# Kernel tuning notes

Measured on AMD Instinct MI355X. Metric: run time of the kernel, lower is better.

## Reference

```python
import jax, jax.numpy as jnp
import numpy as np

N = 50000      # nodes
E = 800000     # edges (no self loops; module re-adds them)
F_IN = 128     # feats_per_node
H1, C1 = 8, 32     # conv1: heads=8, out=32 -> concat hidden = 256
H2, C2 = 1, 128    # conv2: heads=1, out=128, concat=False (mean)
NEG = 0.2      # leaky relu slope


def _glorot(key, shape):
    fan_in, fan_out = shape[-1], int(np.prod(shape[:-1]))
    lim = float(np.sqrt(6.0 / (fan_in + fan_out)))
    return jax.random.uniform(key, shape, jnp.float32, -lim, lim)


def setup_inputs() -> dict:
    key = jax.random.key(0)
    ks = jax.random.split(key, 10)
    x = jax.random.normal(ks[0], (N, F_IN), jnp.float32)
    src = jax.random.randint(ks[1], (E,), 0, N, dtype=jnp.int32)
    off = jax.random.randint(ks[2], (E,), 1, N, dtype=jnp.int32)
    dst = (src + off) % N  # guarantees src != dst (no self loops)
    edge_index = jnp.stack([src, dst])  # [2, E], row0=source j, row1=target i
    return {
        "x": x,
        "edge_index": edge_index,
        "lin1_w": _glorot(ks[3], (H1 * C1, F_IN)),
        "att1_i": _glorot(ks[4], (1, H1, C1)),
        "att1_j": _glorot(ks[5], (1, H1, C1)),
        "bias1": jnp.zeros((H1 * C1,), jnp.float32),
        "lin2_w": _glorot(ks[6], (C2, H1 * C1)),
        "att2_i": _glorot(ks[7], (1, H2, C2)),
        "att2_j": _glorot(ks[8], (1, H2, C2)),
        "bias2": jnp.zeros((C2,), jnp.float32),
    }


def _gat_conv(x, src, dst, lin_w, att_i, att_j, bias, heads, out_ch, concat):
    n = x.shape[0]
    xh = (x @ lin_w.T).reshape(n, heads, out_ch)          # [n, H, C]
    # add self loops (input edges have none; module removes then adds)
    sl = jnp.arange(n, dtype=src.dtype)
    s = jnp.concatenate([src, sl])
    d = jnp.concatenate([dst, sl])
    # per-node attention logits, then gather per edge (avoids per-edge dot)
    ai = jnp.sum(xh * att_i, axis=-1)                     # [n, H]
    aj = jnp.sum(xh * att_j, axis=-1)                     # [n, H]
    alpha = ai[d] + aj[s]                                 # [Etot, H]
    alpha = jnp.where(alpha > 0, alpha, NEG * alpha)      # leaky relu
    # segment softmax over destination node (every node has a self loop)
    m = jax.ops.segment_max(alpha, d, num_segments=n)
    alpha = jnp.exp(alpha - m[d])
    denom = jax.ops.segment_sum(alpha, d, num_segments=n)
    alpha = alpha / (denom[d] + 1e-16)
    # weighted scatter-add aggregation
    out = jax.ops.segment_sum(xh[s] * alpha[:, :, None], d, num_segments=n)
    out = out.reshape(n, heads * out_ch) if concat else out.mean(axis=1)
    return out + bias


def reference(x, edge_index, lin1_w, att1_i, att1_j, bias1,
              lin2_w, att2_i, att2_j, bias2):
    src, dst = edge_index[0], edge_index[1]
    h = _gat_conv(x, src, dst, lin1_w, att1_i, att1_j, bias1, H1, C1, True)
    h = jax.nn.elu(h)
    return _gat_conv(h, src, dst, lin2_w, att2_i, att2_j, bias2, H2, C2, False)
```

## Files before the change

### kernel.cpp

```cpp
#include <hip/hip_runtime.h>
#include <math.h>

#define NN   50000
#define NE   800000
#define FIN  128
#define HID  256
#define NH1  8
#define C2   128
#define CAP  64
#define NEGS 0.2f

#define NGRP 196
#define CAPB 4608
#define NBIN 782

#define W1R  272
#define W2R  144

typedef __attribute__((ext_vector_type(8))) short bf16x8;
typedef __attribute__((ext_vector_type(4))) float f32x4;

__device__ inline unsigned short f2bf(float f) {
    union { float f; unsigned u; } v; v.f = f;
    unsigned u = v.u;
    u += 0x7fffu + ((u >> 16) & 1u);
    return (unsigned short)(u >> 16);
}
__device__ inline float bf2f(unsigned short h) {
    union { unsigned u; float f; } v; v.u = ((unsigned)h) << 16;
    return v.f;
}

__global__ __launch_bounds__(256) void k_bin(const int* __restrict__ ei,
                                             int* __restrict__ gcnt,
                                             int* __restrict__ gbuf,
                                             const float* __restrict__ w1,
                                             const float* __restrict__ w2,
                                             const float* __restrict__ a1i,
                                             const float* __restrict__ a1j,
                                             const float* __restrict__ a2i,
                                             const float* __restrict__ a2j,
                                             unsigned short* __restrict__ w1e,
                                             unsigned short* __restrict__ w2e) {
    const int B = blockIdx.x, t = threadIdx.x;
    if (B < NBIN) {
        __shared__ int hcnt[NGRP], hbase[NGRP], h2[NGRP];
        for (int k = t; k < NGRP; k += 256) { hcnt[k] = 0; h2[k] = 0; }
        __syncthreads();
        int sv[4], bv[4];
#pragma unroll
        for (int u = 0; u < 4; ++u) {
            const int e = B * 1024 + u * 256 + t;
            if (e < NE) {
                const int s = ei[e], d = ei[NE + e];
                sv[u] = s | ((d & 255) << 16);
                bv[u] = d >> 8;
                atomicAdd(&hcnt[bv[u]], 1);
            } else bv[u] = -1;
        }
        __syncthreads();
        for (int k = t; k < NGRP; k += 256)
            if (hcnt[k]) hbase[k] = atomicAdd(&gcnt[k], hcnt[k]);
        __syncthreads();
#pragma unroll
        for (int u = 0; u < 4; ++u) {
            if (bv[u] >= 0) {
                const int lp = atomicAdd(&h2[bv[u]], 1);
                const int pos = hbase[bv[u]] + lp;
                if (pos < CAPB) gbuf[(size_t)bv[u] * CAPB + pos] = sv[u];
            }
        }
    } else if (B < 1038) {
        const int g = (B - NBIN) * 256 + t;
        if (g < 32768) w1e[g] = f2bf(w1[g]);
        else w2e[g - 32768] = f2bf(w2[g - 32768]);
    } else if (B < 1046) {
        const int g = (B - 1038) * 256 + t;
        const int r = g >> 7, k = g & 127;
        const int h = r & 7;
        const float* att = (r < 8) ? a1i : a1j;
        float s = 0.f;
        for (int c = 0; c < 32; ++c)
            s += att[h * 32 + c] * w1[(h * 32 + c) * FIN + k];
        w1e[(256 + r) * FIN + k] = f2bf(s);
    } else if (B < 1048) {
        const int g = (B - 1046) * 256 + t;
        const int r = g >> 8, k = g & 255;
        const float* att = (r == 0) ? a2i : a2j;
        float s = 0.f;
        for (int c = 0; c < C2; ++c)
            s += att[c] * w2[c * HID + k];
        w2e[(128 + r) * HID + k] = f2bf(s);
    } else {
        const int g = (B - 1048) * 256 + t;
        w2e[130 * HID + g] = 0;
    }
}

__global__ __launch_bounds__(256) void k_build(const int* __restrict__ gcnt,
                                               const int* __restrict__ gbuf,
                                               int* __restrict__ cnt,
                                               int* __restrict__ csr) {
    const int g = blockIdx.x, t = threadIdx.x;
    __shared__ int ccnt[256];
    ccnt[t] = 0;
    __syncthreads();
    const int n = min(gcnt[g], CAPB);
    const int64_t base = (int64_t)g * CAPB;
    for (int k0 = 0; k0 < n; k0 += 1024) {
        int vv[4];
#pragma unroll
        for (int u = 0; u < 4; ++u) {
            const int k = k0 + u * 256 + t;
            vv[u] = (k < n) ? gbuf[base + k] : -1;
        }
#pragma unroll
        for (int u = 0; u < 4; ++u) {
            if (vv[u] >= 0) {
                const int s = vv[u] & 0xffff;
                const int dlow = (vv[u] >> 16) & 0xff;
                const int slot = atomicAdd(&ccnt[dlow], 1);
                if (slot < CAP)
                    csr[((size_t)g * 256 + dlow) * CAP + slot] = s;
            }
        }
    }
    __syncthreads();
    const int node = g * 256 + t;
    if (node < NN) cnt[node] = ccnt[t];
}

__global__ __launch_bounds__(512, 4) void k_gemm1(const float* __restrict__ x,
                                                  const unsigned short* __restrict__ wb,
                                                  unsigned short* __restrict__ xh,
                                                  float* __restrict__ ai,
                                                  float* __restrict__ aj) {
    __shared__ unsigned short wl[W1R * FIN];
    const int t = threadIdx.x;
    for (int idx = t; idx < W1R * 16; idx += 512) {
        const int row = idx >> 4, c = idx & 15;
        *(int4*)((char*)wl + row * 256 + ((c ^ (row & 7)) << 4)) =
            *(const int4*)(wb + row * FIN + c * 8);
    }
    __syncthreads();

    const int w = t >> 6, l = t & 63, m = l & 15, q = l >> 4;
    const int arow = blockIdx.x * 128 + w * 16 + m;
    const int rowc = arow < NN ? arow : NN - 1;

    f32x4 acc[17];
#pragma unroll
    for (int nt = 0; nt < 17; ++nt)
#pragma unroll
        for (int b = 0; b < 4; ++b) acc[nt][b] = 0.f;

#pragma unroll
    for (int ks = 0; ks < 4; ++ks) {
        const int k0 = ks * 32 + q * 8;
        const float4 a0 = *(const float4*)(x + (size_t)rowc * FIN + k0);
        const float4 a1 = *(const float4*)(x + (size_t)rowc * FIN + k0 + 4);
        bf16x8 af;
        af[0] = (short)f2bf(a0.x); af[1] = (short)f2bf(a0.y);
        af[2] = (short)f2bf(a0.z); af[3] = (short)f2bf(a0.w);
        af[4] = (short)f2bf(a1.x); af[5] = (short)f2bf(a1.y);
        af[6] = (short)f2bf(a1.z); af[7] = (short)f2bf(a1.w);
        const int cb = ks * 4 + q;
#pragma unroll
        for (int nt = 0; nt < 17; ++nt) {
            const int n = nt * 16 + m;
            const bf16x8 bf = *(const bf16x8*)((const char*)wl + n * 256 + ((cb ^ (n & 7)) << 4));
            acc[nt] = __builtin_amdgcn_mfma_f32_16x16x32_bf16(af, bf, acc[nt], 0, 0, 0);
        }
    }

    const int orow = blockIdx.x * 128 + w * 16 + 4 * q;
#pragma unroll
    for (int b = 0; b < 4; ++b) {
        if (orow + b >= NN) break;
        unsigned short* dst = xh + (size_t)(orow + b) * HID + m;
#pragma unroll
        for (int nt = 0; nt < 16; ++nt) dst[nt * 16] = f2bf(acc[nt][b]);
        if (m < 8) ai[(orow + b) * NH1 + m]       = acc[16][b];
        else       aj[(orow + b) * NH1 + (m - 8)] = acc[16][b];
    }
}

__global__ __launch_bounds__(256) void k_cvt1(const unsigned short* __restrict__ xh,
                                              unsigned char* __restrict__ xq,
                                              float* __restrict__ scl) {
    const int lane = threadIdx.x & 63;
    const int row  = blockIdx.x * 4 + (threadIdx.x >> 6);
    const ushort4 v = ((const ushort4*)(xh + (size_t)row * HID))[lane];
    const float f0 = bf2f(v.x), f1 = bf2f(v.y), f2 = bf2f(v.z), f3 = bf2f(v.w);
    float m = fmaxf(fmaxf(fabsf(f0), fabsf(f1)), fmaxf(fabsf(f2), fabsf(f3)));
#pragma unroll
    for (int off = 1; off < 64; off <<= 1) m = fmaxf(m, __shfl_xor(m, off, 64));
    m = fmaxf(m, 1e-20f);
    const float inv = 127.f / m;
    const int q0 = (int)rintf(f0 * inv) + 128;
    const int q1 = (int)rintf(f1 * inv) + 128;
    const int q2 = (int)rintf(f2 * inv) + 128;
    const int q3 = (int)rintf(f3 * inv) + 128;
    ((unsigned*)(xq + (size_t)row * HID))[lane] =
        (unsigned)q0 | ((unsigned)q1 << 8) | ((unsigned)q2 << 16) | ((unsigned)q3 << 24);
    if (lane == 0) scl[row] = m * (1.f / 127.f);
}

__global__ __launch_bounds__(256) void k_agg1(const unsigned char* __restrict__ xq,
                                              const float* __restrict__ scl,
                                              const unsigned short* __restrict__ xh,
                                              const float* __restrict__ ai,
                                              const float* __restrict__ aj,
                                              const int* __restrict__ cursor,
                                              const int* __restrict__ csr,
                                              const float* __restrict__ bias,
                                              unsigned short* __restrict__ hout) {
    const int lane = threadIdx.x & 63;
    const int i    = blockIdx.x * 4 + (threadIdx.x >> 6);
    const int sub  = lane & 15;
    const int quad = lane >> 4;
    const int myh  = sub >> 1;
    const float a_i = ai[i * NH1 + myh];

    const int deg = min(cursor[i], CAP);
    const int* rowp = csr + (size_t)i * CAP;
    const int svals = (lane < deg) ? rowp[lane] : i;

    float acc[16];
#pragma unroll
    for (int k = 0; k < 16; ++k) acc[k] = 0.f;
    float dsum = 0.f, wsum = 0.f;

    for (int it = 0; it < deg; it += 8) {
#pragma unroll
        for (int u = 0; u < 2; ++u) {
            const int e = it + u * 4 + quad;
            const int s = __shfl(svals, e & 63, 64);
            float aw = a_i + aj[s * NH1 + myh];
            aw = aw > 0.f ? aw : NEGS * aw;
            const float wv = (e < deg) ? __expf(aw) : 0.f;
            dsum += wv;
            const float wvs = wv * scl[s];
            wsum += wvs;
            const int4 raw = ((const int4*)(xq + (size_t)s * HID))[sub];
            const unsigned dx = (unsigned)raw.x, dy = (unsigned)raw.y;
            const unsigned dz = (unsigned)raw.z, dw = (unsigned)raw.w;
            acc[ 0] += wvs * (float)( dx        & 0xffu);
            acc[ 1] += wvs * (float)((dx >>  8) & 0xffu);
            acc[ 2] += wvs * (float)((dx >> 16) & 0xffu);
            acc[ 3] += wvs * (float)( dx >> 24        );
            acc[ 4] += wvs * (float)( dy        & 0xffu);
            acc[ 5] += wvs * (float)((dy >>  8) & 0xffu);
            acc[ 6] += wvs * (float)((dy >> 16) & 0xffu);
            acc[ 7] += wvs * (float)( dy >> 24        );
            acc[ 8] += wvs * (float)( dz        & 0xffu);
            acc[ 9] += wvs * (float)((dz >>  8) & 0xffu);
            acc[10] += wvs * (float)((dz >> 16) & 0xffu);
            acc[11] += wvs * (float)( dz >> 24        );
            acc[12] += wvs * (float)( dw        & 0xffu);
            acc[13] += wvs * (float)((dw >>  8) & 0xffu);
            acc[14] += wvs * (float)((dw >> 16) & 0xffu);
            acc[15] += wvs * (float)( dw >> 24        );
        }
    }
    dsum += __shfl_xor(dsum, 16, 64);
    dsum += __shfl_xor(dsum, 32, 64);
    wsum += __shfl_xor(wsum, 16, 64);
    wsum += __shfl_xor(wsum, 32, 64);
#pragma unroll
    for (int k = 0; k < 16; ++k) {
        acc[k] += __shfl_xor(acc[k], 16, 64);
        acc[k] += __shfl_xor(acc[k], 32, 64);
    }

    float aws = a_i + aj[i * NH1 + myh];
    aws = aws > 0.f ? aws : NEGS * aws;
    const float wself = __expf(aws);
    dsum += wself;
    const ushort4 sv = *(const ushort4*)(xh + (size_t)i * HID + sub * 16 + quad * 4);

    const float inv = 1.f / (dsum + 1e-16f);
    const float c128 = 128.f * wsum;
    const float4 b = ((const float4*)bias)[sub * 4 + quad];
    float4 o;
    o.x = (acc[quad * 4 + 0] - c128 + wself * bf2f(sv.x)) * inv + b.x;
    o.y = (acc[quad * 4 + 1] - c128 + wself * bf2f(sv.y)) * inv + b.y;
    o.z = (acc[quad * 4 + 2] - c128 + wself * bf2f(sv.z)) * inv + b.z;
    o.w = (acc[quad * 4 + 3] - c128 + wself * bf2f(sv.w)) * inv + b.w;
    o.x = o.x > 0.f ? o.x : expm1f(o.x);
    o.y = o.y > 0.f ? o.y : expm1f(o.y);
    o.z = o.z > 0.f ? o.z : expm1f(o.z);
    o.w = o.w > 0.f ? o.w : expm1f(o.w);
    ushort4 ov;
    ov.x = f2bf(o.x); ov.y = f2bf(o.y); ov.z = f2bf(o.z); ov.w = f2bf(o.w);
    ((ushort4*)(hout + (size_t)i * HID))[sub * 4 + quad] = ov;
}

__global__ __launch_bounds__(512, 4) void k_gemm2(const unsigned short* __restrict__ h1,
                                                  const unsigned short* __restrict__ wb,
                                                  unsigned short* __restrict__ xh2,
                                                  float* __restrict__ ai2,
                                                  float* __restrict__ aj2) {
    __shared__ unsigned short wl[W2R * HID];
    const int t = threadIdx.x;
    for (int idx = t; idx < W2R * 32; idx += 512) {
        const int row = idx >> 5, c = idx & 31;
        *(int4*)((char*)wl + row * 512 + ((c ^ (row & 7)) << 4)) =
            *(const int4*)(wb + row * HID + c * 8);
    }
    __syncthreads();

    const int w = t >> 6, l = t & 63, m = l & 15, q = l >> 4;
    const int arow = blockIdx.x * 128 + w * 16 + m;
    const int rowc = arow < NN ? arow : NN - 1;

    f32x4 acc[9];
#pragma unroll
    for (int nt = 0; nt < 9; ++nt)
#pragma unroll
        for (int b = 0; b < 4; ++b) acc[nt][b] = 0.f;

#pragma unroll
    for (int ks = 0; ks < 8; ++ks) {
        const int k0 = ks * 32 + q * 8;
        const bf16x8 af = *(const bf16x8*)(h1 + (size_t)rowc * HID + k0);
        const int cb = ks * 4 + q;
#pragma unroll
        for (int nt = 0; nt < 9; ++nt) {
            const int n = nt * 16 + m;
            const bf16x8 bf = *(const bf16x8*)((const char*)wl + n * 512 + ((cb ^ (n & 7)) << 4));
            acc[nt] = __builtin_amdgcn_mfma_f32_16x16x32_bf16(af, bf, acc[nt], 0, 0, 0);
        }
    }

    const int orow = blockIdx.x * 128 + w * 16 + 4 * q;
#pragma unroll
    for (int b = 0; b < 4; ++b) {
        if (orow + b >= NN) break;
        unsigned short* dst = xh2 + (size_t)(orow + b) * C2 + m;
#pragma unroll
        for (int nt = 0; nt < 8; ++nt) dst[nt * 16] = f2bf(acc[nt][b]);
        if (m == 0) ai2[orow + b] = acc[8][b];
        if (m == 1) aj2[orow + b] = acc[8][b];
    }
}

__global__ __launch_bounds__(256) void k_cvt2(const unsigned short* __restrict__ xh2,
                                              unsigned char* __restrict__ xq2,
                                              float* __restrict__ scl2) {
    const int lane = threadIdx.x & 63;
    const int row  = blockIdx.x * 4 + (threadIdx.x >> 6);
    const ushort2 v = ((const ushort2*)(xh2 + (size_t)row * C2))[lane];
    const float f0 = bf2f(v.x), f1 = bf2f(v.y);
    float m = fmaxf(fabsf(f0), fabsf(f1));
#pragma unroll
    for (int off = 1; off < 64; off <<= 1) m = fmaxf(m, __shfl_xor(m, off, 64));
    m = fmaxf(m, 1e-20f);
    const float inv = 127.f / m;
    const int q0 = (int)rintf(f0 * inv) + 128;
    const int q1 = (int)rintf(f1 * inv) + 128;
    ((unsigned short*)(xq2 + (size_t)row * C2))[lane] =
        (unsigned short)(q0 | (q1 << 8));
    if (lane == 0) scl2[row] = m * (1.f / 127.f);
}

__global__ __launch_bounds__(256) void k_agg2(const unsigned char* __restrict__ xq2,
                                              const float* __restrict__ scl2,
                                              const unsigned short* __restrict__ xh2,
                                              const float* __restrict__ ai2v,
                                              const float* __restrict__ aj2v,
                                              const int* __restrict__ cursor,
                                              const int* __restrict__ csr,
                                              const float* __restrict__ bias,
                                              float* __restrict__ out) {
    const int lane = threadIdx.x & 63;
    const int i    = blockIdx.x * 4 + (threadIdx.x >> 6);
    const int sub  = lane & 7;
    const int oct  = lane >> 3;
    const float a_i = ai2v[i];

    const int deg = min(cursor[i], CAP);
    const int* rowp = csr + (size_t)i * CAP;
    const int svals = (lane < deg) ? rowp[lane] : i;

    float acc[16];
#pragma unroll
    for (int k = 0; k < 16; ++k) acc[k] = 0.f;
    float dsum = 0.f, wsum = 0.f;

    for (int it = 0; it < deg; it += 16) {
#pragma unroll
        for (int u = 0; u < 2; ++u) {
            const int e = it + u * 8 + oct;
            const int s = __shfl(svals, e & 63, 64);
            float aw = a_i + aj2v[s];
            aw = aw > 0.f ? aw : NEGS * aw;
            const float wv = (e < deg) ? __expf(aw) : 0.f;
            dsum += wv;
            const float wvs = wv * scl2[s];
            wsum += wvs;
            const int4 raw = ((const int4*)(xq2 + (size_t)s * C2))[sub];
            const unsigned dx = (unsigned)raw.x, dy = (unsigned)raw.y;
            const unsigned dz = (unsigned)raw.z, dw = (unsigned)raw.w;
            acc[ 0] += wvs * (float)( dx        & 0xffu);
            acc[ 1] += wvs * (float)((dx >>  8) & 0xffu);
            acc[ 2] += wvs * (float)((dx >> 16) & 0xffu);
            acc[ 3] += wvs * (float)( dx >> 24        );
            acc[ 4] += wvs * (float)( dy        & 0xffu);
            acc[ 5] += wvs * (float)((dy >>  8) & 0xffu);
            acc[ 6] += wvs * (float)((dy >> 16) & 0xffu);
            acc[ 7] += wvs * (float)( dy >> 24        );
            acc[ 8] += wvs * (float)( dz        & 0xffu);
            acc[ 9] += wvs * (float)((dz >>  8) & 0xffu);
            acc[10] += wvs * (float)((dz >> 16) & 0xffu);
            acc[11] += wvs * (float)( dz >> 24        );
            acc[12] += wvs * (float)( dw        & 0xffu);
            acc[13] += wvs * (float)((dw >>  8) & 0xffu);
            acc[14] += wvs * (float)((dw >> 16) & 0xffu);
            acc[15] += wvs * (float)( dw >> 24        );
        }
    }
    dsum += __shfl_xor(dsum, 8, 64);
    dsum += __shfl_xor(dsum, 16, 64);
    dsum += __shfl_xor(dsum, 32, 64);
    wsum += __shfl_xor(wsum, 8, 64);
    wsum += __shfl_xor(wsum, 16, 64);
    wsum += __shfl_xor(wsum, 32, 64);
#pragma unroll
    for (int k = 0; k < 16; ++k) {
        acc[k] += __shfl_xor(acc[k], 8, 64);
        acc[k] += __shfl_xor(acc[k], 16, 64);
        acc[k] += __shfl_xor(acc[k], 32, 64);
    }

    float aws = a_i + aj2v[i];
    aws = aws > 0.f ? aws : NEGS * aws;
    const float wself = __expf(aws);
    dsum += wself;
    const ushort2 sv = *(const ushort2*)(xh2 + (size_t)i * C2 + sub * 16 + oct * 2);

    const float inv = 1.f / (dsum + 1e-16f);
    const float c128 = 128.f * wsum;
    const float2 b = ((const float2*)bias)[sub * 8 + oct];
    float2 o;
    o.x = (acc[oct * 2 + 0] - c128 + wself * bf2f(sv.x)) * inv + b.x;
    o.y = (acc[oct * 2 + 1] - c128 + wself * bf2f(sv.y)) * inv + b.y;
    ((float2*)(out + (size_t)i * C2))[sub * 8 + oct] = o;
}

extern "C" void kernel_launch(void* const* d_in, const int* in_sizes, int n_in,
                              void* d_out, int out_size, void* d_ws, size_t ws_size,
                              hipStream_t stream) {
    const float* x      = (const float*)d_in[0];
    const int*   ei     = (const int*)  d_in[1];
    const float* lin1_w = (const float*)d_in[2];
    const float* att1_i = (const float*)d_in[3];
    const float* att1_j = (const float*)d_in[4];
    const float* bias1  = (const float*)d_in[5];
    const float* lin2_w = (const float*)d_in[6];
    const float* att2_i = (const float*)d_in[7];
    const float* att2_j = (const float*)d_in[8];
    const float* bias2  = (const float*)d_in[9];
    float* out = (float*)d_out;

    char* wsb = (char*)d_ws;
    size_t off = 0;
    auto alloc = [&](size_t bytes) -> void* {
        void* p = wsb + off;
        off += (bytes + 255) & ~(size_t)255;
        return p;
    };
    int*            gcnt   = (int*)           alloc((size_t)NGRP * 4);
    int*            gbuf   = (int*)           alloc((size_t)NGRP * CAPB * 4);
    int*            cnt    = (int*)           alloc((size_t)NN * 4);
    int*            csr    = (int*)           alloc((size_t)NN * CAP * 4);
    unsigned short* w1e    = (unsigned short*)alloc((size_t)W1R * FIN * 2);
    unsigned short* w2e    = (unsigned short*)alloc((size_t)W2R * HID * 2);
    unsigned short* xh1    = (unsigned short*)alloc((size_t)NN * HID * 2);
    unsigned char*  xq1    = (unsigned char*) alloc((size_t)NN * HID);
    float*          scl1   = (float*)         alloc((size_t)NN * 4);
    float*          ai1    = (float*)         alloc((size_t)NN * NH1 * 4);
    float*          aj1    = (float*)         alloc((size_t)NN * NH1 * 4);
    unsigned short* h1     = (unsigned short*)alloc((size_t)NN * HID * 2);
    unsigned short* xh2    = (unsigned short*)alloc((size_t)NN * C2 * 2);
    unsigned char*  xq2    = (unsigned char*) alloc((size_t)NN * C2);
    float*          scl2   = (float*)         alloc((size_t)NN * 4);
    float*          ai2    = (float*)         alloc((size_t)NN * 4);
    float*          aj2    = (float*)         alloc((size_t)NN * 4);
    if (off > ws_size) return;

    const int gm = (NN + 127) / 128;
    hipMemsetAsync(gcnt, 0, (size_t)NGRP * 4, stream);
    k_bin<<<1062, 256, 0, stream>>>(ei, gcnt, gbuf, lin1_w, lin2_w,
                                    att1_i, att1_j, att2_i, att2_j, w1e, w2e);
    k_build<<<NGRP, 256, 0, stream>>>(gcnt, gbuf, cnt, csr);
    k_gemm1<<<gm, 512, 0, stream>>>(x, w1e, xh1, ai1, aj1);
    k_cvt1<<<NN / 4, 256, 0, stream>>>(xh1, xq1, scl1);
    k_agg1<<<NN / 4, 256, 0, stream>>>(xq1, scl1, xh1, ai1, aj1, cnt, csr, bias1, h1);
    k_gemm2<<<gm, 512, 0, stream>>>(h1, w2e, xh2, ai2, aj2);
    k_cvt2<<<NN / 4, 256, 0, stream>>>(xh2, xq2, scl2);
    k_agg2<<<NN / 4, 256, 0, stream>>>(xq2, scl2, xh2, ai2, aj2, cnt, csr, bias2, out);
}
```

Measured before the change: 169.3 us.

## Fuse int8 quantization into GEMM epilogues and precompute per-edge attention weights in LDS

The two GEMM kernels now remap their output columns so each lane holds a contiguous slice of a row. The epilogue then computes the row max, the bf16 copy and the int8 quantization in place, which removes the separate k_cvt1/k_cvt2 passes and their extra read of xh. The aggregation kernels compute the exp attention weights per edge once, all heads at once, and store them in shared memory, so the inner loop no longer does redundant gathers and exps. The inner loop also uses packed two-wide FMAs. The costs are LDS use, a new swizzle to avoid bank conflicts, and more register pressure in the GEMM epilogue.

```diff
diff --git a/kernel.cpp b/kernel.cpp
--- a/kernel.cpp
+++ b/kernel.cpp
@@ -17,8 +17,11 @@
 #define W1R  272
 #define W2R  144
 
+#define SWZ(n) ((((n) & 7)) ^ (((n) >> 4) & 7))
+
 typedef __attribute__((ext_vector_type(8))) short bf16x8;
 typedef __attribute__((ext_vector_type(4))) float f32x4;
+typedef __attribute__((ext_vector_type(2))) float f32x2;
 
 __device__ inline unsigned short f2bf(float f) {
     union { float f; unsigned u; } v; v.f = f;
@@ -133,13 +136,15 @@
 __global__ __launch_bounds__(512, 4) void k_gemm1(const float* __restrict__ x,
                                                   const unsigned short* __restrict__ wb,
                                                   unsigned short* __restrict__ xh,
+                                                  unsigned char* __restrict__ xq,
+                                                  float* __restrict__ scl,
                                                   float* __restrict__ ai,
                                                   float* __restrict__ aj) {
     __shared__ unsigned short wl[W1R * FIN];
     const int t = threadIdx.x;
     for (int idx = t; idx < W1R * 16; idx += 512) {
         const int row = idx >> 4, c = idx & 15;
-        *(int4*)((char*)wl + row * 256 + ((c ^ (row & 7)) << 4)) =
+        *(int4*)((char*)wl + row * 256 + ((c ^ SWZ(row)) << 4)) =
             *(const int4*)(wb + row * FIN + c * 8);
     }
     __syncthreads();
@@ -167,8 +172,8 @@
         const int cb = ks * 4 + q;
 #pragma unroll
         for (int nt = 0; nt < 17; ++nt) {
-            const int n = nt * 16 + m;
-            const bf16x8 bf = *(const bf16x8*)((const char*)wl + n * 256 + ((cb ^ (n & 7)) << 4));
+            const int n = (nt < 16) ? (m * 16 + nt) : (256 + m);
+            const bf16x8 bf = *(const bf16x8*)((const char*)wl + n * 256 + ((cb ^ SWZ(n)) << 4));
             acc[nt] = __builtin_amdgcn_mfma_f32_16x16x32_bf16(af, bf, acc[nt], 0, 0, 0);
         }
     }
@@ -177,33 +182,34 @@
 #pragma unroll
     for (int b = 0; b < 4; ++b) {
         if (orow + b >= NN) break;
-        unsigned short* dst = xh + (size_t)(orow + b) * HID + m;
-#pragma unroll
-        for (int nt = 0; nt < 16; ++nt) dst[nt * 16] = f2bf(acc[nt][b]);
-        if (m < 8) ai[(orow + b) * NH1 + m]       = acc[16][b];
-        else       aj[(orow + b) * NH1 + (m - 8)] = acc[16][b];
-    }
-}
-
-__global__ __launch_bounds__(256) void k_cvt1(const unsigned short* __restrict__ xh,
-                                              unsigned char* __restrict__ xq,
-                                              float* __restrict__ scl) {
-    const int lane = threadIdx.x & 63;
-    const int row  = blockIdx.x * 4 + (threadIdx.x >> 6);
-    const ushort4 v = ((const ushort4*)(xh + (size_t)row * HID))[lane];
-    const float f0 = bf2f(v.x), f1 = bf2f(v.y), f2 = bf2f(v.z), f3 = bf2f(v.w);
-    float m = fmaxf(fmaxf(fabsf(f0), fabsf(f1)), fmaxf(fabsf(f2), fabsf(f3)));
-#pragma unroll
-    for (int off = 1; off < 64; off <<= 1) m = fmaxf(m, __shfl_xor(m, off, 64));
-    m = fmaxf(m, 1e-20f);
-    const float inv = 127.f / m;
-    const int q0 = (int)rintf(f0 * inv) + 128;
-    const int q1 = (int)rintf(f1 * inv) + 128;
-    const int q2 = (int)rintf(f2 * inv) + 128;
-    const int q3 = (int)rintf(f3 * inv) + 128;
-    ((unsigned*)(xq + (size_t)row * HID))[lane] =
-        (unsigned)q0 | ((unsigned)q1 << 8) | ((unsigned)q2 << 16) | ((unsigned)q3 << 24);
-    if (lane == 0) scl[row] = m * (1.f / 127.f);
+        const int row = orow + b;
+        float mx = 1e-20f;
+#pragma unroll
+        for (int nt = 0; nt < 16; ++nt) mx = fmaxf(mx, fabsf(acc[nt][b]));
+#pragma unroll
+        for (int off = 1; off < 16; off <<= 1) mx = fmaxf(mx, __shfl_xor(mx, off, 16));
+        const float qsc = 127.f / mx;
+        unsigned bw[8];
+#pragma unroll
+        for (int k = 0; k < 8; ++k)
+            bw[k] = (unsigned)f2bf(acc[2 * k][b]) | ((unsigned)f2bf(acc[2 * k + 1][b]) << 16);
+        int4* bd = (int4*)(xh + (size_t)row * HID + m * 16);
+        bd[0] = make_int4(bw[0], bw[1], bw[2], bw[3]);
+        bd[1] = make_int4(bw[4], bw[5], bw[6], bw[7]);
+        unsigned qw[4];
+#pragma unroll
+        for (int k = 0; k < 4; ++k) {
+            const int q0 = (int)rintf(acc[4 * k + 0][b] * qsc) + 128;
+            const int q1 = (int)rintf(acc[4 * k + 1][b] * qsc) + 128;
+            const int q2 = (int)rintf(acc[4 * k + 2][b] * qsc) + 128;
+            const int q3 = (int)rintf(acc[4 * k + 3][b] * qsc) + 128;
+            qw[k] = (unsigned)q0 | ((unsigned)q1 << 8) | ((unsigned)q2 << 16) | ((unsigned)q3 << 24);
+        }
+        *(int4*)(xq + (size_t)row * HID + m * 16) = make_int4(qw[0], qw[1], qw[2], qw[3]);
+        if (m == 0) scl[row] = mx * (1.f / 127.f);
+        if (m < 8) ai[row * NH1 + m]       = acc[16][b];
+        else       aj[row * NH1 + (m - 8)] = acc[16][b];
+    }
 }
 
 __global__ __launch_bounds__(256) void k_agg1(const unsigned char* __restrict__ xq,
@@ -211,24 +217,49 @@
                                               const unsigned short* __restrict__ xh,
                                               const float* __restrict__ ai,
                                               const float* __restrict__ aj,
-                                              const int* __restrict__ cursor,
+                                              const int* __restrict__ cnt,
                                               const int* __restrict__ csr,
                                               const float* __restrict__ bias,
                                               unsigned short* __restrict__ hout) {
+    __shared__ float2 psh[4][80 * 8];
+    const int wid  = threadIdx.x >> 6;
     const int lane = threadIdx.x & 63;
-    const int i    = blockIdx.x * 4 + (threadIdx.x >> 6);
+    const int i    = blockIdx.x * 4 + wid;
     const int sub  = lane & 15;
     const int quad = lane >> 4;
     const int myh  = sub >> 1;
-    const float a_i = ai[i * NH1 + myh];
-
-    const int deg = min(cursor[i], CAP);
+
+    const int deg = min(cnt[i], CAP);
     const int* rowp = csr + (size_t)i * CAP;
     const int svals = (lane < deg) ? rowp[lane] : i;
 
-    float acc[16];
-#pragma unroll
-    for (int k = 0; k < 16; ++k) acc[k] = 0.f;
+    float2* wl = psh[wid];
+    {
+        const float4 ai0 = ((const float4*)ai)[i * 2];
+        const float4 ai1 = ((const float4*)ai)[i * 2 + 1];
+        const float4 aj0 = ((const float4*)aj)[svals * 2];
+        const float4 aj1 = ((const float4*)aj)[svals * 2 + 1];
+        const float sc = scl[svals];
+        const float vm = (lane < deg) ? 1.f : 0.f;
+        float a, wv;
+        a = ai0.x + aj0.x; a = a > 0.f ? a : NEGS * a; wv = vm * __expf(a); wl[lane * 8 + 0] = make_float2(wv, wv * sc);
+        a = ai0.y + aj0.y; a = a > 0.f ? a : NEGS * a; wv = vm * __expf(a); wl[lane * 8 + 1] = make_float2(wv, wv * sc);
+        a = ai0.z + aj0.z; a = a > 0.f ? a : NEGS * a; wv = vm * __expf(a); wl[lane * 8 + 2] = make_float2(wv, wv * sc);
+        a = ai0.w + aj0.w; a = a > 0.f ? a : NEGS * a; wv = vm * __expf(a); wl[lane * 8 + 3] = make_float2(wv, wv * sc);
+        a = ai1.x + aj1.x; a = a > 0.f ? a : NEGS * a; wv = vm * __expf(a); wl[lane * 8 + 4] = make_float2(wv, wv * sc);
+        a = ai1.y + aj1.y; a = a > 0.f ? a : NEGS * a; wv = vm * __expf(a); wl[lane * 8 + 5] = make_float2(wv, wv * sc);
+        a = ai1.z + aj1.z; a = a > 0.f ? a : NEGS * a; wv = vm * __expf(a); wl[lane * 8 + 6] = make_float2(wv, wv * sc);
+        a = ai1.w + aj1.w; a = a > 0.f ? a : NEGS * a; wv = vm * __expf(a); wl[lane * 8 + 7] = make_float2(wv, wv * sc);
+        if (lane < 16) {
+            float2* zp = wl + (64 + lane) * 8;
+#pragma unroll
+            for (int h = 0; h < 8; ++h) zp[h] = make_float2(0.f, 0.f);
+        }
+    }
+
+    f32x2 acc2[8];
+#pragma unroll
+    for (int k = 0; k < 8; ++k) acc2[k] = (f32x2){0.f, 0.f};
     float dsum = 0.f, wsum = 0.f;
 
     for (int it = 0; it < deg; it += 8) {
@@ -236,44 +267,37 @@
         for (int u = 0; u < 2; ++u) {
             const int e = it + u * 4 + quad;
             const int s = __shfl(svals, e & 63, 64);
-            float aw = a_i + aj[s * NH1 + myh];
-            aw = aw > 0.f ? aw : NEGS * aw;
-            const float wv = (e < deg) ? __expf(aw) : 0.f;
-            dsum += wv;
-            const float wvs = wv * scl[s];
-            wsum += wvs;
+            const float2 wp = wl[e * 8 + myh];
+            dsum += wp.x; wsum += wp.y;
+            const f32x2 pv = {wp.y, wp.y};
             const int4 raw = ((const int4*)(xq + (size_t)s * HID))[sub];
             const unsigned dx = (unsigned)raw.x, dy = (unsigned)raw.y;
             const unsigned dz = (unsigned)raw.z, dw = (unsigned)raw.w;
-            acc[ 0] += wvs * (float)( dx        & 0xffu);
-            acc[ 1] += wvs * (float)((dx >>  8) & 0xffu);
-            acc[ 2] += wvs * (float)((dx >> 16) & 0xffu);
-            acc[ 3] += wvs * (float)( dx >> 24        );
-            acc[ 4] += wvs * (float)( dy        & 0xffu);
-            acc[ 5] += wvs * (float)((dy >>  8) & 0xffu);
-            acc[ 6] += wvs * (float)((dy >> 16) & 0xffu);
-            acc[ 7] += wvs * (float)( dy >> 24        );
-            acc[ 8] += wvs * (float)( dz        & 0xffu);
-            acc[ 9] += wvs * (float)((dz >>  8) & 0xffu);
-            acc[10] += wvs * (float)((dz >> 16) & 0xffu);
-            acc[11] += wvs * (float)( dz >> 24        );
-            acc[12] += wvs * (float)( dw        & 0xffu);
-            acc[13] += wvs * (float)((dw >>  8) & 0xffu);
-            acc[14] += wvs * (float)((dw >> 16) & 0xffu);
-            acc[15] += wvs * (float)( dw >> 24        );
+            f32x2 d;
+            d = (f32x2){(float)(dx & 0xffu), (float)((dx >> 8) & 0xffu)};   acc2[0] = pv * d + acc2[0];
+            d = (f32x2){(float)((dx >> 16) & 0xffu), (float)(dx >> 24)};   acc2[1] = pv * d + acc2[1];
+            d = (f32x2){(float)(dy & 0xffu), (float)((dy >> 8) & 0xffu)};   acc2[2] = pv * d + acc2[2];
+            d = (f32x2){(float)((dy >> 16) & 0xffu), (float)(dy >> 24)};   acc2[3] = pv * d + acc2[3];
+            d = (f32x2){(float)(dz & 0xffu), (float)((dz >> 8) & 0xffu)};   acc2[4] = pv * d + acc2[4];
+            d = (f32x2){(float)((dz >> 16) & 0xffu), (float)(dz >> 24)};   acc2[5] = pv * d + acc2[5];
+            d = (f32x2){(float)(dw & 0xffu), (float)((dw >> 8) & 0xffu)};   acc2[6] = pv * d + acc2[6];
+            d = (f32x2){(float)((dw >> 16) & 0xffu), (float)(dw >> 24)};   acc2[7] = pv * d + acc2[7];
         }
     }
     dsum += __shfl_xor(dsum, 16, 64);
     dsum += __shfl_xor(dsum, 32, 64);
     wsum += __shfl_xor(wsum, 16, 64);
     wsum += __shfl_xor(wsum, 32, 64);
-#pragma unroll
-    for (int k = 0; k < 16; ++k) {
-        acc[k] += __shfl_xor(acc[k], 16, 64);
-        acc[k] += __shfl_xor(acc[k], 32, 64);
-    }
-
-    float aws = a_i + aj[i * NH1 + myh];
+    float accf[16];
+#pragma unroll
+    for (int k = 0; k < 8; ++k) {
+        float x0 = acc2[k].x, x1 = acc2[k].y;
+        x0 += __shfl_xor(x0, 16, 64); x0 += __shfl_xor(x0, 32, 64);
+        x1 += __shfl_xor(x1, 16, 64); x1 += __shfl_xor(x1, 32, 64);
+        accf[2 * k] = x0; accf[2 * k + 1] = x1;
+    }
+
+    float aws = ai[i * NH1 + myh] + aj[i * NH1 + myh];
     aws = aws > 0.f ? aws : NEGS * aws;
     const float wself = __expf(aws);
     dsum += wself;
@@ -283,10 +307,10 @@
     const float c128 = 128.f * wsum;
     const float4 b = ((const float4*)bias)[sub * 4 + quad];
     float4 o;
-    o.x = (acc[quad * 4 + 0] - c128 + wself * bf2f(sv.x)) * inv + b.x;
-    o.y = (acc[quad * 4 + 1] - c128 + wself * bf2f(sv.y)) * inv + b.y;
-    o.z = (acc[quad * 4 + 2] - c128 + wself * bf2f(sv.z)) * inv + b.z;
-    o.w = (acc[quad * 4 + 3] - c128 + wself * bf2f(sv.w)) * inv + b.w;
+    o.x = (accf[quad * 4 + 0] - c128 + wself * bf2f(sv.x)) * inv + b.x;
+    o.y = (accf[quad * 4 + 1] - c128 + wself * bf2f(sv.y)) * inv + b.y;
+    o.z = (accf[quad * 4 + 2] - c128 + wself * bf2f(sv.z)) * inv + b.z;
+    o.w = (accf[quad * 4 + 3] - c128 + wself * bf2f(sv.w)) * inv + b.w;
     o.x = o.x > 0.f ? o.x : expm1f(o.x);
     o.y = o.y > 0.f ? o.y : expm1f(o.y);
     o.z = o.z > 0.f ? o.z : expm1f(o.z);
@@ -299,13 +323,15 @@
 __global__ __launch_bounds__(512, 4) void k_gemm2(const unsigned short* __restrict__ h1,
                                                   const unsigned short* __restrict__ wb,
                                                   unsigned short* __restrict__ xh2,
+                                                  unsigned char* __restrict__ xq2,
+                                                  float* __restrict__ scl2,
                                                   float* __restrict__ ai2,
                                                   float* __restrict__ aj2) {
     __shared__ unsigned short wl[W2R * HID];
     const int t = threadIdx.x;
     for (int idx = t; idx < W2R * 32; idx += 512) {
         const int row = idx >> 5, c = idx & 31;
-        *(int4*)((char*)wl + row * 512 + ((c ^ (row & 7)) << 4)) =
+        *(int4*)((char*)wl + row * 512 + ((c ^ SWZ(row)) << 4)) =
             *(const int4*)(wb + row * HID + c * 8);
     }
     __syncthreads();
@@ -327,8 +353,8 @@
         const int cb = ks * 4 + q;
 #pragma unroll
         for (int nt = 0; nt < 9; ++nt) {
-            const int n = nt * 16 + m;
-            const bf16x8 bf = *(const bf16x8*)((const char*)wl + n * 512 + ((cb ^ (n & 7)) << 4));
+            const int n = (nt < 8) ? (m * 8 + nt) : (128 + m);
+            const bf16x8 bf = *(const bf16x8*)((const char*)wl + n * 512 + ((cb ^ SWZ(n)) << 4));
             acc[nt] = __builtin_amdgcn_mfma_f32_16x16x32_bf16(af, bf, acc[nt], 0, 0, 0);
         }
     }
@@ -337,31 +363,32 @@
 #pragma unroll
     for (int b = 0; b < 4; ++b) {
         if (orow + b >= NN) break;
-        unsigned short* dst = xh2 + (size_t)(orow + b) * C2 + m;
-#pragma unroll
-        for (int nt = 0; nt < 8; ++nt) dst[nt * 16] = f2bf(acc[nt][b]);
-        if (m == 0) ai2[orow + b] = acc[8][b];
-        if (m == 1) aj2[orow + b] = acc[8][b];
-    }
-}
-
-__global__ __launch_bounds__(256) void k_cvt2(const unsigned short* __restrict__ xh2,
-                                              unsigned char* __restrict__ xq2,
-                                              float* __restrict__ scl2) {
-    const int lane = threadIdx.x & 63;
-    const int row  = blockIdx.x * 4 + (threadIdx.x >> 6);
-    const ushort2 v = ((const ushort2*)(xh2 + (size_t)row * C2))[lane];
-    const float f0 = bf2f(v.x), f1 = bf2f(v.y);
-    float m = fmaxf(fabsf(f0), fabsf(f1));
-#pragma unroll
-    for (int off = 1; off < 64; off <<= 1) m = fmaxf(m, __shfl_xor(m, off, 64));
-    m = fmaxf(m, 1e-20f);
-    const float inv = 127.f / m;
-    const int q0 = (int)rintf(f0 * inv) + 128;
-    const int q1 = (int)rintf(f1 * inv) + 128;
-    ((unsigned short*)(xq2 + (size_t)row * C2))[lane] =
-        (unsigned short)(q0 | (q1 << 8));
-    if (lane == 0) scl2[row] = m * (1.f / 127.f);
+        const int row = orow + b;
+        float mx = 1e-20f;
+#pragma unroll
+        for (int nt = 0; nt < 8; ++nt) mx = fmaxf(mx, fabsf(acc[nt][b]));
+#pragma unroll
+        for (int off = 1; off < 16; off <<= 1) mx = fmaxf(mx, __shfl_xor(mx, off, 16));
+        const float qsc = 127.f / mx;
+        unsigned bw[4];
+#pragma unroll
+        for (int k = 0; k < 4; ++k)
+            bw[k] = (unsigned)f2bf(acc[2 * k][b]) | ((unsigned)f2bf(acc[2 * k + 1][b]) << 16);
+        *(int4*)(xh2 + (size_t)row * C2 + m * 8) = make_int4(bw[0], bw[1], bw[2], bw[3]);
+        unsigned qw[2];
+#pragma unroll
+        for (int k = 0; k < 2; ++k) {
+            const int q0 = (int)rintf(acc[4 * k + 0][b] * qsc) + 128;
+            const int q1 = (int)rintf(acc[4 * k + 1][b] * qsc) + 128;
+            const int q2 = (int)rintf(acc[4 * k + 2][b] * qsc) + 128;
+            const int q3 = (int)rintf(acc[4 * k + 3][b] * qsc) + 128;
+            qw[k] = (unsigned)q0 | ((unsigned)q1 << 8) | ((unsigned)q2 << 16) | ((unsigned)q3 << 24);
+        }
+        *(int2*)(xq2 + (size_t)row * C2 + m * 8) = make_int2(qw[0], qw[1]);
+        if (m == 0) scl2[row] = mx * (1.f / 127.f);
+        if (m == 0) ai2[row] = acc[8][b];
+        if (m == 1) aj2[row] = acc[8][b];
+    }
 }
 
 __global__ __launch_bounds__(256) void k_agg2(const unsigned char* __restrict__ xq2,
@@ -369,23 +396,34 @@
                                               const unsigned short* __restrict__ xh2,
                                               const float* __restrict__ ai2v,
                                               const float* __restrict__ aj2v,
-                                              const int* __restrict__ cursor,
+                                              const int* __restrict__ cnt,
                                               const int* __restrict__ csr,
                                               const float* __restrict__ bias,
                                               float* __restrict__ out) {
+    __shared__ float2 psh[4][80];
+    const int wid  = threadIdx.x >> 6;
     const int lane = threadIdx.x & 63;
-    const int i    = blockIdx.x * 4 + (threadIdx.x >> 6);
+    const int i    = blockIdx.x * 4 + wid;
     const int sub  = lane & 7;
     const int oct  = lane >> 3;
     const float a_i = ai2v[i];
 
-    const int deg = min(cursor[i], CAP);
+    const int deg = min(cnt[i], CAP);
     const int* rowp = csr + (size_t)i * CAP;
     const int svals = (lane < deg) ? rowp[lane] : i;
 
-    float acc[16];
-#pragma unroll
-    for (int k = 0; k < 16; ++k) acc[k] = 0.f;
+    float2* wl = psh[wid];
+    {
+        float a = a_i + aj2v[svals];
+        a = a > 0.f ? a : NEGS * a;
+        const float wv = (lane < deg) ? __expf(a) : 0.f;
+        wl[lane] = make_float2(wv, wv * scl2[svals]);
+        if (lane < 16) wl[64 + lane] = make_float2(0.f, 0.f);
+    }
+
+    f32x2 acc2[8];
+#pragma unroll
+    for (int k = 0; k < 8; ++k) acc2[k] = (f32x2){0.f, 0.f};
     float dsum = 0.f, wsum = 0.f;
 
     for (int it = 0; it < deg; it += 16) {
@@ -393,31 +431,21 @@
         for (int u = 0; u < 2; ++u) {
             const int e = it + u * 8 + oct;
             const int s = __shfl(svals, e & 63, 64);
-            float aw = a_i + aj2v[s];
-            aw = aw > 0.f ? aw : NEGS * aw;
-            const float wv = (e < deg) ? __expf(aw) : 0.f;
-            dsum += wv;
-            const float wvs = wv * scl2[s];
-            wsum += wvs;
+            const float2 wp = wl[e];
+            dsum += wp.x; wsum += wp.y;
+            const f32x2 pv = {wp.y, wp.y};
             const int4 raw = ((const int4*)(xq2 + (size_t)s * C2))[sub];
             const unsigned dx = (unsigned)raw.x, dy = (unsigned)raw.y;
             const unsigned dz = (unsigned)raw.z, dw = (unsigned)raw.w;
-            acc[ 0] += wvs * (float)( dx        & 0xffu);
-            acc[ 1] += wvs * (float)((dx >>  8) & 0xffu);
-            acc[ 2] += wvs * (float)((dx >> 16) & 0xffu);
-            acc[ 3] += wvs * (float)( dx >> 24        );
-            acc[ 4] += wvs * (float)( dy        & 0xffu);
-            acc[ 5] += wvs * (float)((dy >>  8) & 0xffu);
-            acc[ 6] += wvs * (float)((dy >> 16) & 0xffu);
-            acc[ 7] += wvs * (float)( dy >> 24        );
-            acc[ 8] += wvs * (float)( dz        & 0xffu);
-            acc[ 9] += wvs * (float)((dz >>  8) & 0xffu);
-            acc[10] += wvs * (float)((dz >> 16) & 0xffu);
-            acc[11] += wvs * (float)( dz >> 24        );
-            acc[12] += wvs * (float)( dw        & 0xffu);
-            acc[13] += wvs * (float)((dw >>  8) & 0xffu);
-            acc[14] += wvs * (float)((dw >> 16) & 0xffu);
-            acc[15] += wvs * (float)( dw >> 24        );
+            f32x2 d;
+            d = (f32x2){(float)(dx & 0xffu), (float)((dx >> 8) & 0xffu)};   acc2[0] = pv * d + acc2[0];
+            d = (f32x2){(float)((dx >> 16) & 0xffu), (float)(dx >> 24)};   acc2[1] = pv * d + acc2[1];
+            d = (f32x2){(float)(dy & 0xffu), (float)((dy >> 8) & 0xffu)};   acc2[2] = pv * d + acc2[2];
+            d = (f32x2){(float)((dy >> 16) & 0xffu), (float)(dy >> 24)};   acc2[3] = pv * d + acc2[3];
+            d = (f32x2){(float)(dz & 0xffu), (float)((dz >> 8) & 0xffu)};   acc2[4] = pv * d + acc2[4];
+            d = (f32x2){(float)((dz >> 16) & 0xffu), (float)(dz >> 24)};   acc2[5] = pv * d + acc2[5];
+            d = (f32x2){(float)(dw & 0xffu), (float)((dw >> 8) & 0xffu)};   acc2[6] = pv * d + acc2[6];
+            d = (f32x2){(float)((dw >> 16) & 0xffu), (float)(dw >> 24)};   acc2[7] = pv * d + acc2[7];
         }
     }
     dsum += __shfl_xor(dsum, 8, 64);
@@ -426,11 +454,13 @@
     wsum += __shfl_xor(wsum, 8, 64);
     wsum += __shfl_xor(wsum, 16, 64);
     wsum += __shfl_xor(wsum, 32, 64);
-#pragma unroll
-    for (int k = 0; k < 16; ++k) {
-        acc[k] += __shfl_xor(acc[k], 8, 64);
-        acc[k] += __shfl_xor(acc[k], 16, 64);
-        acc[k] += __shfl_xor(acc[k], 32, 64);
+    float accf[16];
+#pragma unroll
+    for (int k = 0; k < 8; ++k) {
+        float x0 = acc2[k].x, x1 = acc2[k].y;
+        x0 += __shfl_xor(x0, 8, 64); x0 += __shfl_xor(x0, 16, 64); x0 += __shfl_xor(x0, 32, 64);
+        x1 += __shfl_xor(x1, 8, 64); x1 += __shfl_xor(x1, 16, 64); x1 += __shfl_xor(x1, 32, 64);
+        accf[2 * k] = x0; accf[2 * k + 1] = x1;
     }
 
     float aws = a_i + aj2v[i];
@@ -443,8 +473,8 @@
     const float c128 = 128.f * wsum;
     const float2 b = ((const float2*)bias)[sub * 8 + oct];
     float2 o;
-    o.x = (acc[oct * 2 + 0] - c128 + wself * bf2f(sv.x)) * inv + b.x;
-    o.y = (acc[oct * 2 + 1] - c128 + wself * bf2f(sv.y)) * inv + b.y;
+    o.x = (accf[oct * 2 + 0] - c128 + wself * bf2f(sv.x)) * inv + b.x;
+    o.y = (accf[oct * 2 + 1] - c128 + wself * bf2f(sv.y)) * inv + b.y;
     ((float2*)(out + (size_t)i * C2))[sub * 8 + oct] = o;
 }
 
@@ -494,10 +524,8 @@
     k_bin<<<1062, 256, 0, stream>>>(ei, gcnt, gbuf, lin1_w, lin2_w,
                                     att1_i, att1_j, att2_i, att2_j, w1e, w2e);
     k_build<<<NGRP, 256, 0, stream>>>(gcnt, gbuf, cnt, csr);
-    k_gemm1<<<gm, 512, 0, stream>>>(x, w1e, xh1, ai1, aj1);
-    k_cvt1<<<NN / 4, 256, 0, stream>>>(xh1, xq1, scl1);
+    k_gemm1<<<gm, 512, 0, stream>>>(x, w1e, xh1, xq1, scl1, ai1, aj1);
     k_agg1<<<NN / 4, 256, 0, stream>>>(xq1, scl1, xh1, ai1, aj1, cnt, csr, bias1, h1);
-    k_gemm2<<<gm, 512, 0, stream>>>(h1, w2e, xh2, ai2, aj2);
-    k_cvt2<<<NN / 4, 256, 0, stream>>>(xh2, xq2, scl2);
+    k_gemm2<<<gm, 512, 0, stream>>>(h1, w2e, xh2, xq2, scl2, ai2, aj2);
     k_agg2<<<NN / 4, 256, 0, stream>>>(xq2, scl2, xh2, ai2, aj2, cnt, csr, bias2, out);
 }
```

Measured after the change: 179.9 us. 6.3% more time.

## Fuse int8 row quantization into GEMM epilogues and remap output columns

Applied to the files above, without the earlier changes.

Folds the separate per-row int8 quantization kernels (k_cvt1, k_cvt2) into the epilogues of both GEMMs. The B-column mapping is permuted so that each lane owns a contiguous 16- or 8-wide chunk of the output row, which allows vectorized int4 stores of bf16 and int8 data. The swizzle is extended to keep LDS reads free of bank conflicts under the new mapping. This removes two kernel launches and a full re-read of the bf16 features, at the cost of more epilogue work and register pressure in the GEMM kernels.

```diff
diff --git a/kernel.cpp b/kernel.cpp
--- a/kernel.cpp
+++ b/kernel.cpp
@@ -16,6 +16,8 @@
 
 #define W1R  272
 #define W2R  144
+
+#define SWZ(n) ((((n) & 7)) ^ (((n) >> 4) & 7))
 
 typedef __attribute__((ext_vector_type(8))) short bf16x8;
 typedef __attribute__((ext_vector_type(4))) float f32x4;
@@ -133,13 +135,15 @@
 __global__ __launch_bounds__(512, 4) void k_gemm1(const float* __restrict__ x,
                                                   const unsigned short* __restrict__ wb,
                                                   unsigned short* __restrict__ xh,
+                                                  unsigned char* __restrict__ xq,
+                                                  float* __restrict__ scl,
                                                   float* __restrict__ ai,
                                                   float* __restrict__ aj) {
     __shared__ unsigned short wl[W1R * FIN];
     const int t = threadIdx.x;
     for (int idx = t; idx < W1R * 16; idx += 512) {
         const int row = idx >> 4, c = idx & 15;
-        *(int4*)((char*)wl + row * 256 + ((c ^ (row & 7)) << 4)) =
+        *(int4*)((char*)wl + row * 256 + ((c ^ SWZ(row)) << 4)) =
             *(const int4*)(wb + row * FIN + c * 8);
     }
     __syncthreads();
@@ -167,8 +171,8 @@
         const int cb = ks * 4 + q;
 #pragma unroll
         for (int nt = 0; nt < 17; ++nt) {
-            const int n = nt * 16 + m;
-            const bf16x8 bf = *(const bf16x8*)((const char*)wl + n * 256 + ((cb ^ (n & 7)) << 4));
+            const int n = (nt < 16) ? (m * 16 + nt) : (256 + m);
+            const bf16x8 bf = *(const bf16x8*)((const char*)wl + n * 256 + ((cb ^ SWZ(n)) << 4));
             acc[nt] = __builtin_amdgcn_mfma_f32_16x16x32_bf16(af, bf, acc[nt], 0, 0, 0);
         }
     }
@@ -177,33 +181,34 @@
 #pragma unroll
     for (int b = 0; b < 4; ++b) {
         if (orow + b >= NN) break;
-        unsigned short* dst = xh + (size_t)(orow + b) * HID + m;
-#pragma unroll
-        for (int nt = 0; nt < 16; ++nt) dst[nt * 16] = f2bf(acc[nt][b]);
-        if (m < 8) ai[(orow + b) * NH1 + m]       = acc[16][b];
-        else       aj[(orow + b) * NH1 + (m - 8)] = acc[16][b];
-    }
-}
-
-__global__ __launch_bounds__(256) void k_cvt1(const unsigned short* __restrict__ xh,
-                                              unsigned char* __restrict__ xq,
-                                              float* __restrict__ scl) {
-    const int lane = threadIdx.x & 63;
-    const int row  = blockIdx.x * 4 + (threadIdx.x >> 6);
-    const ushort4 v = ((const ushort4*)(xh + (size_t)row * HID))[lane];
-    const float f0 = bf2f(v.x), f1 = bf2f(v.y), f2 = bf2f(v.z), f3 = bf2f(v.w);
-    float m = fmaxf(fmaxf(fabsf(f0), fabsf(f1)), fmaxf(fabsf(f2), fabsf(f3)));
-#pragma unroll
-    for (int off = 1; off < 64; off <<= 1) m = fmaxf(m, __shfl_xor(m, off, 64));
-    m = fmaxf(m, 1e-20f);
-    const float inv = 127.f / m;
-    const int q0 = (int)rintf(f0 * inv) + 128;
-    const int q1 = (int)rintf(f1 * inv) + 128;
-    const int q2 = (int)rintf(f2 * inv) + 128;
-    const int q3 = (int)rintf(f3 * inv) + 128;
-    ((unsigned*)(xq + (size_t)row * HID))[lane] =
-        (unsigned)q0 | ((unsigned)q1 << 8) | ((unsigned)q2 << 16) | ((unsigned)q3 << 24);
-    if (lane == 0) scl[row] = m * (1.f / 127.f);
+        const int row = orow + b;
+        float mx = 1e-20f;
+#pragma unroll
+        for (int nt = 0; nt < 16; ++nt) mx = fmaxf(mx, fabsf(acc[nt][b]));
+#pragma unroll
+        for (int off = 1; off < 16; off <<= 1) mx = fmaxf(mx, __shfl_xor(mx, off, 16));
+        const float qsc = 127.f / mx;
+        unsigned bw[8];
+#pragma unroll
+        for (int k = 0; k < 8; ++k)
+            bw[k] = (unsigned)f2bf(acc[2 * k][b]) | ((unsigned)f2bf(acc[2 * k + 1][b]) << 16);
+        int4* bd = (int4*)(xh + (size_t)row * HID + m * 16);
+        bd[0] = make_int4(bw[0], bw[1], bw[2], bw[3]);
+        bd[1] = make_int4(bw[4], bw[5], bw[6], bw[7]);
+        unsigned qw[4];
+#pragma unroll
+        for (int k = 0; k < 4; ++k) {
+            const int q0 = (int)rintf(acc[4 * k + 0][b] * qsc) + 128;
+            const int q1 = (int)rintf(acc[4 * k + 1][b] * qsc) + 128;
+            const int q2 = (int)rintf(acc[4 * k + 2][b] * qsc) + 128;
+            const int q3 = (int)rintf(acc[4 * k + 3][b] * qsc) + 128;
+            qw[k] = (unsigned)q0 | ((unsigned)q1 << 8) | ((unsigned)q2 << 16) | ((unsigned)q3 << 24);
+        }
+        *(int4*)(xq + (size_t)row * HID + m * 16) = make_int4(qw[0], qw[1], qw[2], qw[3]);
+        if (m == 0) scl[row] = mx * (1.f / 127.f);
+        if (m < 8) ai[row * NH1 + m]       = acc[16][b];
+        else       aj[row * NH1 + (m - 8)] = acc[16][b];
+    }
 }
 
 __global__ __launch_bounds__(256) void k_agg1(const unsigned char* __restrict__ xq,
@@ -211,7 +216,7 @@
                                               const unsigned short* __restrict__ xh,
                                               const float* __restrict__ ai,
                                               const float* __restrict__ aj,
-                                              const int* __restrict__ cursor,
+                                              const int* __restrict__ cnt,
                                               const int* __restrict__ csr,
                                               const float* __restrict__ bias,
                                               unsigned short* __restrict__ hout) {
@@ -222,7 +227,7 @@
     const int myh  = sub >> 1;
     const float a_i = ai[i * NH1 + myh];
 
-    const int deg = min(cursor[i], CAP);
+    const int deg = min(cnt[i], CAP);
     const int* rowp = csr + (size_t)i * CAP;
     const int svals = (lane < deg) ? rowp[lane] : i;
 
@@ -299,13 +304,15 @@
 __global__ __launch_bounds__(512, 4) void k_gemm2(const unsigned short* __restrict__ h1,
                                                   const unsigned short* __restrict__ wb,
                                                   unsigned short* __restrict__ xh2,
+                                                  unsigned char* __restrict__ xq2,
+                                                  float* __restrict__ scl2,
                                                   float* __restrict__ ai2,
                                                   float* __restrict__ aj2) {
     __shared__ unsigned short wl[W2R * HID];
     const int t = threadIdx.x;
     for (int idx = t; idx < W2R * 32; idx += 512) {
         const int row = idx >> 5, c = idx & 31;
-        *(int4*)((char*)wl + row * 512 + ((c ^ (row & 7)) << 4)) =
+        *(int4*)((char*)wl + row * 512 + ((c ^ SWZ(row)) << 4)) =
             *(const int4*)(wb + row * HID + c * 8);
     }
     __syncthreads();
@@ -327,8 +334,8 @@
         const int cb = ks * 4 + q;
 #pragma unroll
         for (int nt = 0; nt < 9; ++nt) {
-            const int n = nt * 16 + m;
-            const bf16x8 bf = *(const bf16x8*)((const char*)wl + n * 512 + ((cb ^ (n & 7)) << 4));
+            const int n = (nt < 8) ? (m * 8 + nt) : (128 + m);
+            const bf16x8 bf = *(const bf16x8*)((const char*)wl + n * 512 + ((cb ^ SWZ(n)) << 4));
             acc[nt] = __builtin_amdgcn_mfma_f32_16x16x32_bf16(af, bf, acc[nt], 0, 0, 0);
         }
     }
@@ -337,31 +344,32 @@
 #pragma unroll
     for (int b = 0; b < 4; ++b) {
         if (orow + b >= NN) break;
-        unsigned short* dst = xh2 + (size_t)(orow + b) * C2 + m;
-#pragma unroll
-        for (int nt = 0; nt < 8; ++nt) dst[nt * 16] = f2bf(acc[nt][b]);
-        if (m == 0) ai2[orow + b] = acc[8][b];
-        if (m == 1) aj2[orow + b] = acc[8][b];
-    }
-}
-
-__global__ __launch_bounds__(256) void k_cvt2(const unsigned short* __restrict__ xh2,
-                                              unsigned char* __restrict__ xq2,
-                                              float* __restrict__ scl2) {
-    const int lane = threadIdx.x & 63;
-    const int row  = blockIdx.x * 4 + (threadIdx.x >> 6);
-    const ushort2 v = ((const ushort2*)(xh2 + (size_t)row * C2))[lane];
-    const float f0 = bf2f(v.x), f1 = bf2f(v.y);
-    float m = fmaxf(fabsf(f0), fabsf(f1));
-#pragma unroll
-    for (int off = 1; off < 64; off <<= 1) m = fmaxf(m, __shfl_xor(m, off, 64));
-    m = fmaxf(m, 1e-20f);
-    const float inv = 127.f / m;
-    const int q0 = (int)rintf(f0 * inv) + 128;
-    const int q1 = (int)rintf(f1 * inv) + 128;
-    ((unsigned short*)(xq2 + (size_t)row * C2))[lane] =
-        (unsigned short)(q0 | (q1 << 8));
-    if (lane == 0) scl2[row] = m * (1.f / 127.f);
+        const int row = orow + b;
+        float mx = 1e-20f;
+#pragma unroll
+        for (int nt = 0; nt < 8; ++nt) mx = fmaxf(mx, fabsf(acc[nt][b]));
+#pragma unroll
+        for (int off = 1; off < 16; off <<= 1) mx = fmaxf(mx, __shfl_xor(mx, off, 16));
+        const float qsc = 127.f / mx;
+        unsigned bw[4];
+#pragma unroll
+        for (int k = 0; k < 4; ++k)
+            bw[k] = (unsigned)f2bf(acc[2 * k][b]) | ((unsigned)f2bf(acc[2 * k + 1][b]) << 16);
+        *(int4*)(xh2 + (size_t)row * C2 + m * 8) = make_int4(bw[0], bw[1], bw[2], bw[3]);
+        unsigned qw[2];
+#pragma unroll
+        for (int k = 0; k < 2; ++k) {
+            const int q0 = (int)rintf(acc[4 * k + 0][b] * qsc) + 128;
+            const int q1 = (int)rintf(acc[4 * k + 1][b] * qsc) + 128;
+            const int q2 = (int)rintf(acc[4 * k + 2][b] * qsc) + 128;
+            const int q3 = (int)rintf(acc[4 * k + 3][b] * qsc) + 128;
+            qw[k] = (unsigned)q0 | ((unsigned)q1 << 8) | ((unsigned)q2 << 16) | ((unsigned)q3 << 24);
+        }
+        *(int2*)(xq2 + (size_t)row * C2 + m * 8) = make_int2(qw[0], qw[1]);
+        if (m == 0) scl2[row] = mx * (1.f / 127.f);
+        if (m == 0) ai2[row] = acc[8][b];
+        if (m == 1) aj2[row] = acc[8][b];
+    }
 }
 
 __global__ __launch_bounds__(256) void k_agg2(const unsigned char* __restrict__ xq2,
@@ -369,7 +377,7 @@
                                               const unsigned short* __restrict__ xh2,
                                               const float* __restrict__ ai2v,
                                               const float* __restrict__ aj2v,
-                                              const int* __restrict__ cursor,
+                                              const int* __restrict__ cnt,
                                               const int* __restrict__ csr,
                                               const float* __restrict__ bias,
                                               float* __restrict__ out) {
@@ -379,7 +387,7 @@
     const int oct  = lane >> 3;
     const float a_i = ai2v[i];
 
-    const int deg = min(cursor[i], CAP);
+    const int deg = min(cnt[i], CAP);
     const int* rowp = csr + (size_t)i * CAP;
     const int svals = (lane < deg) ? rowp[lane] : i;
 
@@ -494,10 +502,8 @@
     k_bin<<<1062, 256, 0, stream>>>(ei, gcnt, gbuf, lin1_w, lin2_w,
                                     att1_i, att1_j, att2_i, att2_j, w1e, w2e);
     k_build<<<NGRP, 256, 0, stream>>>(gcnt, gbuf, cnt, csr);
-    k_gemm1<<<gm, 512, 0, stream>>>(x, w1e, xh1, ai1, aj1);
-    k_cvt1<<<NN / 4, 256, 0, stream>>>(xh1, xq1, scl1);
+    k_gemm1<<<gm, 512, 0, stream>>>(x, w1e, xh1, xq1, scl1, ai1, aj1);
     k_agg1<<<NN / 4, 256, 0, stream>>>(xq1, scl1, xh1, ai1, aj1, cnt, csr, bias1, h1);
-    k_gemm2<<<gm, 512, 0, stream>>>(h1, w2e, xh2, ai2, aj2);
-    k_cvt2<<<NN / 4, 256, 0, stream>>>(xh2, xq2, scl2);
+    k_gemm2<<<gm, 512, 0, stream>>>(h1, w2e, xh2, xq2, scl2, ai2, aj2);
     k_agg2<<<NN / 4, 256, 0, stream>>>(xq2, scl2, xh2, ai2, aj2, cnt, csr, bias2, out);
 }
```

Measured after the change: 154.9 us. 8.5% less time.
